# Kernel tuning notes

Hardware: AMD Instinct MI355X
Metric: run time of the kernel (lower is better)

The kernel has to match this reference:

```python
import jax, jax.numpy as jnp
import numpy as np

N = 50000      # nodes
E = 800000     # edges
D_IN, D_H, D_OUT = 256, 256, 128
BN_EPS = 1e-5


def setup_inputs() -> dict:
    key = jax.random.key(0)
    ks = jax.random.split(key, 16)
    inp = {}
    inp["x"] = jax.random.normal(ks[0], (N, D_IN), dtype=jnp.float32)
    inp["edge_index"] = jax.random.randint(ks[1], (2, E), 0, N, dtype=jnp.int32)
    s1 = 1.0 / np.sqrt(D_IN)
    s2 = 1.0 / np.sqrt(D_H)
    inp["W1"] = jax.random.normal(ks[2], (D_IN, D_H), dtype=jnp.float32) * s1
    inp["b1"] = jnp.zeros((D_H,), dtype=jnp.float32)
    inp["g1"] = jnp.ones((D_H,), dtype=jnp.float32)
    inp["be1"] = jnp.zeros((D_H,), dtype=jnp.float32)
    inp["m1"] = jax.random.normal(ks[3], (D_H,), dtype=jnp.float32) * 0.1
    inp["v1"] = jax.random.uniform(ks[4], (D_H,), dtype=jnp.float32, minval=0.5, maxval=1.5)
    inp["W2"] = jax.random.normal(ks[5], (D_H, D_H), dtype=jnp.float32) * s2
    inp["b2"] = jnp.zeros((D_H,), dtype=jnp.float32)
    inp["g2"] = jnp.ones((D_H,), dtype=jnp.float32)
    inp["be2"] = jnp.zeros((D_H,), dtype=jnp.float32)
    inp["m2"] = jax.random.normal(ks[6], (D_H,), dtype=jnp.float32) * 0.1
    inp["v2"] = jax.random.uniform(ks[7], (D_H,), dtype=jnp.float32, minval=0.5, maxval=1.5)
    inp["W3"] = jax.random.normal(ks[8], (D_H, D_OUT), dtype=jnp.float32) * s2
    inp["b3"] = jnp.zeros((D_OUT,), dtype=jnp.float32)
    return inp


def reference(x, edge_index, W1, b1, g1, be1, m1, v1,
              W2, b2, g2, be2, m2, v2, W3, b3):
    # Add self-loops (PyG GCNConv default) and compute symmetric normalization once.
    loop = jnp.arange(N, dtype=edge_index.dtype)
    src = jnp.concatenate([edge_index[0], loop])   # [E+N]
    dst = jnp.concatenate([edge_index[1], loop])   # [E+N]
    deg = jax.ops.segment_sum(jnp.ones_like(dst, dtype=x.dtype), dst, num_segments=N)
    dinv = jax.lax.rsqrt(deg)                      # deg >= 1 thanks to self-loops
    norm = (dinv[src] * dinv[dst])[:, None]        # [E+N, 1]

    def gcn_conv(h, W, b):
        h = h @ W                                   # [N, D]
        agg = jax.ops.segment_sum(h[src] * norm, dst, num_segments=N)
        return agg + b

    def bn_eval(h, g, be, m, v):
        return (h - m) * (g * jax.lax.rsqrt(v + BN_EPS)) + be

    h = jax.nn.relu(bn_eval(gcn_conv(x, W1, b1), g1, be1, m1, v1))  # dropout = identity (eval)
    h = jax.nn.relu(bn_eval(gcn_conv(h, W2, b2), g2, be2, m2, v2))
    out = gcn_conv(h, W3, b3)                       # [N, D_OUT]
    return out
```

## Files before the change

kernel.cpp:

```cpp
#include <hip/hip_runtime.h>
#include <hip/hip_bf16.h>
#include <hip/hip_fp16.h>


#define GN 50000
#define GE 800000

typedef float f32x4 __attribute__((ext_vector_type(4)));
typedef short bf16x8 __attribute__((ext_vector_type(8)));

static __device__ __forceinline__ ushort f2bf_rn(float f) {
    unsigned u = __float_as_uint(f);
    u += 0x7fffu + ((u >> 16) & 1u);
    return (ushort)(u >> 16);
}
static __device__ __forceinline__ float bf2f(ushort h) {
    return __uint_as_float(((unsigned)h) << 16);
}


__global__ __launch_bounds__(256) void init_kernel(int* counts, int* cursor) {
    int i = blockIdx.x * 256 + threadIdx.x;
    if (i < GN) { counts[i] = 0; cursor[i] = 0; }
}

__global__ __launch_bounds__(256) void count_kernel(const int* __restrict__ dst, int* __restrict__ counts) {
    int e = blockIdx.x * 256 + threadIdx.x;
    if (e < GE) atomicAdd(&counts[dst[e]], 1);
}

__global__ __launch_bounds__(256) void dinv_kernel(const int* __restrict__ counts, float* __restrict__ dinv) {
    int i = blockIdx.x * 256 + threadIdx.x;
    if (i < GN) dinv[i] = rsqrtf((float)counts[i] + 1.0f);
}

__global__ __launch_bounds__(1024) void scan_kernel(const int* __restrict__ counts, int* __restrict__ row_ptr) {
    __shared__ int sums[1024];
    int tid = threadIdx.x;
    int chunk = (GN + 1023) / 1024;
    int start = tid * chunk;
    int end = min(start + chunk, GN);
    int s = 0;
    for (int i = start; i < end; i++) s += counts[i];
    sums[tid] = s;
    __syncthreads();
    for (int off = 1; off < 1024; off <<= 1) {
        int v = (tid >= off) ? sums[tid - off] : 0;
        __syncthreads();
        sums[tid] += v;
        __syncthreads();
    }
    int run = (tid == 0) ? 0 : sums[tid - 1];
    for (int i = start; i < end; i++) { row_ptr[i] = run; run += counts[i]; }
    if (tid == 1023) row_ptr[GN] = sums[1023];
}

__global__ __launch_bounds__(256) void fill_kernel(const int* __restrict__ src, const int* __restrict__ dst,
                                                   const int* __restrict__ row_ptr, int* __restrict__ cursor,
                                                   int* __restrict__ col) {
    int e = blockIdx.x * 256 + threadIdx.x;
    if (e < GE) {
        int d = dst[e];
        int pos = row_ptr[d] + atomicAdd(&cursor[d], 1);
        col[pos] = src[e];
    }
}

__global__ __launch_bounds__(256) void params_kernel(
    const float* b1, const float* g1, const float* be1, const float* m1, const float* v1,
    const float* b2, const float* g2, const float* be2, const float* m2, const float* v2,
    float* prm) {
    int t = threadIdx.x;
    float s1 = g1[t] * rsqrtf(v1[t] + 1e-5f);
    prm[0 * 256 + t] = s1;
    prm[1 * 256 + t] = (b1[t] - m1[t]) * s1 + be1[t];
    float s2 = g2[t] * rsqrtf(v2[t] + 1e-5f);
    prm[2 * 256 + t] = s2;
    prm[3 * 256 + t] = (b2[t] - m2[t]) * s2 + be2[t];
}


__global__ __launch_bounds__(256) void conv_split(const float* __restrict__ in, ushort* __restrict__ hi,
                                                  ushort* __restrict__ lo, int n4) {
    int i = blockIdx.x * 256 + threadIdx.x;
    if (i >= n4) return;
    float4 v = *(const float4*)&in[(size_t)i * 4];
    ushort4 h, l;
    h.x = f2bf_rn(v.x); l.x = f2bf_rn(v.x - bf2f(h.x));
    h.y = f2bf_rn(v.y); l.y = f2bf_rn(v.y - bf2f(h.y));
    h.z = f2bf_rn(v.z); l.z = f2bf_rn(v.z - bf2f(h.z));
    h.w = f2bf_rn(v.w); l.w = f2bf_rn(v.w - bf2f(h.w));
    *(ushort4*)&hi[(size_t)i * 4] = h;
    *(ushort4*)&lo[(size_t)i * 4] = l;
}

__global__ __launch_bounds__(256) void transpose_w(const float* __restrict__ W, ushort* __restrict__ hiT,
                                                   ushort* __restrict__ loT, int DO) {
    int idx = blockIdx.x * 256 + threadIdx.x;
    if (idx >= DO * 256) return;
    int n = idx >> 8, k = idx & 255;
    float v = W[k * DO + n];
    ushort h = f2bf_rn(v);
    hiT[idx] = h;
    loT[idx] = f2bf_rn(v - bf2f(h));
}


template <int DO>
__global__ __launch_bounds__(256) void gemm_mfma(const ushort* __restrict__ Ahi, const ushort* __restrict__ Alo,
                                                 const ushort* __restrict__ Bhi, const ushort* __restrict__ Blo,
                                                 const float* __restrict__ dinv, __half* __restrict__ C, int M) {
    __shared__ ushort lds[4][128][40];
    int tid = threadIdx.x;
    int lane = tid & 63;
    int wave = tid >> 6;
    int wm = wave >> 1, wn = wave & 1;
    int m0 = blockIdx.x * 128;
    int n0 = blockIdx.y * 128;
    int rsel = lane & 15;
    int ksel = (lane >> 4) * 8;

    f32x4 acc[4][4] = {};

    for (int k0 = 0; k0 < 256; k0 += 32) {
        auto stage = [&](const ushort* __restrict__ src, int baseRow, int rClamp, int p) {
#pragma unroll
            for (int j = 0; j < 2; j++) {
                int o = (tid + j * 256) * 16;
                int row = o >> 6;
                int kb = o & 63;
                int rg = min(baseRow + row, rClamp);
                uint4 v = *(const uint4*)((const char*)src + (size_t)rg * 512 + (size_t)k0 * 2 + kb);
                *(uint4*)((char*)&lds[p][row][0] + kb) = v;
            }
        };
        stage(Ahi, m0, M - 1, 0);
        stage(Alo, m0, M - 1, 1);
        stage(Bhi, n0, DO - 1, 2);
        stage(Blo, n0, DO - 1, 3);
        __syncthreads();

        bf16x8 bh[4], bl[4];
#pragma unroll
        for (int ni = 0; ni < 4; ni++) {
            bh[ni] = *(const bf16x8*)&lds[2][wn * 64 + ni * 16 + rsel][ksel];
            bl[ni] = *(const bf16x8*)&lds[3][wn * 64 + ni * 16 + rsel][ksel];
        }
#pragma unroll
        for (int mi = 0; mi < 4; mi++) {
            bf16x8 ah = *(const bf16x8*)&lds[0][wm * 64 + mi * 16 + rsel][ksel];
            bf16x8 al = *(const bf16x8*)&lds[1][wm * 64 + mi * 16 + rsel][ksel];
#pragma unroll
            for (int ni = 0; ni < 4; ni++) {
                acc[mi][ni] = __builtin_amdgcn_mfma_f32_16x16x32_bf16(ah, bh[ni], acc[mi][ni], 0, 0, 0);
                acc[mi][ni] = __builtin_amdgcn_mfma_f32_16x16x32_bf16(ah, bl[ni], acc[mi][ni], 0, 0, 0);
                acc[mi][ni] = __builtin_amdgcn_mfma_f32_16x16x32_bf16(al, bh[ni], acc[mi][ni], 0, 0, 0);
            }
        }
        __syncthreads();
    }

#pragma unroll
    for (int mi = 0; mi < 4; mi++) {
#pragma unroll
        for (int j = 0; j < 4; j++) {
            int r = m0 + wm * 64 + mi * 16 + (lane >> 4) * 4 + j;
            if (r < M) {
                float dv = dinv[r];
#pragma unroll
                for (int ni = 0; ni < 4; ni++) {
                    int c = n0 + wn * 64 + ni * 16 + rsel;
                    C[(size_t)r * DO + c] = __float2half_rn(acc[mi][ni][j] * dv);
                }
            }
        }
    }
}

template <int D, int MODE>
__global__ __launch_bounds__(256) void agg_kernel(const __half* __restrict__ Hs, const int* __restrict__ row_ptr,
                                                  const int* __restrict__ col, const float* __restrict__ dinv,
                                                  const float* __restrict__ pa, const float* __restrict__ pc,
                                                  float* __restrict__ outF, ushort* __restrict__ outHi,
                                                  ushort* __restrict__ outLo, int M) {
    constexpr int V = D / 64;
    int w = blockIdx.x * 4 + (threadIdx.x >> 6);
    if (w >= M) return;
    int lane = threadIdx.x & 63;
    const __half* base = Hs + lane * V;
    float acc[V];

    auto addrow = [&](const __half* p) {
        if constexpr (V == 4) {
            __half2 v01 = *(const __half2*)(p);
            __half2 v23 = *(const __half2*)(p + 2);
            float2 f0 = __half22float2(v01);
            float2 f1 = __half22float2(v23);
            acc[0] += f0.x; acc[1] += f0.y; acc[2] += f1.x; acc[3] += f1.y;
        } else {
            __half2 v01 = *(const __half2*)(p);
            float2 f0 = __half22float2(v01);
            acc[0] += f0.x; acc[1] += f0.y;
        }
    };
#pragma unroll
    for (int j = 0; j < V; j++) acc[j] = 0.f;
    addrow(base + (size_t)w * D);

    int e = row_ptr[w], end = row_ptr[w + 1];
    for (; e + 4 <= end; e += 4) {
        int s0 = col[e + 0], s1 = col[e + 1], s2 = col[e + 2], s3 = col[e + 3];
        addrow(base + (size_t)s0 * D);
        addrow(base + (size_t)s1 * D);
        addrow(base + (size_t)s2 * D);
        addrow(base + (size_t)s3 * D);
    }
    for (; e < end; e++) addrow(base + (size_t)col[e] * D);

    float dv = dinv[w];
    if constexpr (MODE == 1) {
        ushort4 h, l;
        float val;
        int d = lane * V;
        val = fmaxf(fmaf(acc[0] * dv, pa[d + 0], pc[d + 0]), 0.f);
        h.x = f2bf_rn(val); l.x = f2bf_rn(val - bf2f(h.x));
        val = fmaxf(fmaf(acc[1] * dv, pa[d + 1], pc[d + 1]), 0.f);
        h.y = f2bf_rn(val); l.y = f2bf_rn(val - bf2f(h.y));
        val = fmaxf(fmaf(acc[2] * dv, pa[d + 2], pc[d + 2]), 0.f);
        h.z = f2bf_rn(val); l.z = f2bf_rn(val - bf2f(h.z));
        val = fmaxf(fmaf(acc[3] * dv, pa[d + 3], pc[d + 3]), 0.f);
        h.w = f2bf_rn(val); l.w = f2bf_rn(val - bf2f(h.w));
        *(ushort4*)&outHi[(size_t)w * D + d] = h;
        *(ushort4*)&outLo[(size_t)w * D + d] = l;
    } else {
#pragma unroll
        for (int j = 0; j < V; j++) {
            int d = lane * V + j;
            outF[(size_t)w * D + d] = acc[j] * dv + pa[d];
        }
    }
}


extern "C" void kernel_launch(void* const* d_in, const int* in_sizes, int n_in,
                              void* d_out, int out_size, void* d_ws, size_t ws_size,
                              hipStream_t stream) {
    const float* x = (const float*)d_in[0];
    const int* ei = (const int*)d_in[1];
    const int* srcIdx = ei;
    const int* dstIdx = ei + GE;
    const float* W1 = (const float*)d_in[2];
    const float* b1 = (const float*)d_in[3];
    const float* g1 = (const float*)d_in[4];
    const float* be1 = (const float*)d_in[5];
    const float* m1 = (const float*)d_in[6];
    const float* v1 = (const float*)d_in[7];
    const float* W2 = (const float*)d_in[8];
    const float* b2 = (const float*)d_in[9];
    const float* g2 = (const float*)d_in[10];
    const float* be2 = (const float*)d_in[11];
    const float* m2 = (const float*)d_in[12];
    const float* v2 = (const float*)d_in[13];
    const float* W3 = (const float*)d_in[14];
    const float* b3 = (const float*)d_in[15];
    float* out = (float*)d_out;

    size_t off = 0;
    char* wsb = (char*)d_ws;
    auto take = [&](size_t bytes) -> char* {
        char* p = wsb + off;
        off += (bytes + 255) & ~(size_t)255;
        return p;
    };
    float* dinv = (float*)take((size_t)GN * 4);
    int* counts = (int*)take((size_t)GN * 4);
    int* cursor = (int*)take((size_t)GN * 4);
    int* row_ptr = (int*)take((size_t)(GN + 1) * 4);
    int* col = (int*)take((size_t)GE * 4);
    float* prm = (float*)take(4 * 256 * 4);
    __half* hH = (__half*)take((size_t)GN * 256 * 2);
    ushort* Phi = (ushort*)take((size_t)GN * 256 * 2);
    ushort* Plo = (ushort*)take((size_t)GN * 256 * 2);
    ushort* WT1h = (ushort*)take(256 * 256 * 2);
    ushort* WT1l = (ushort*)take(256 * 256 * 2);
    ushort* WT2h = (ushort*)take(256 * 256 * 2);
    ushort* WT2l = (ushort*)take(256 * 256 * 2);
    ushort* WT3h = (ushort*)take(128 * 256 * 2);
    ushort* WT3l = (ushort*)take(128 * 256 * 2);

    const float* a1 = prm + 0 * 256;
    const float* c1 = prm + 1 * 256;
    const float* a2 = prm + 2 * 256;
    const float* c2 = prm + 3 * 256;

    int nb = (GN + 255) / 256;
    int eb = (GE + 255) / 256;

    init_kernel<<<nb, 256, 0, stream>>>(counts, cursor);
    count_kernel<<<eb, 256, 0, stream>>>(dstIdx, counts);
    dinv_kernel<<<nb, 256, 0, stream>>>(counts, dinv);
    scan_kernel<<<1, 1024, 0, stream>>>(counts, row_ptr);
    fill_kernel<<<eb, 256, 0, stream>>>(srcIdx, dstIdx, row_ptr, cursor, col);
    params_kernel<<<1, 256, 0, stream>>>(b1, g1, be1, m1, v1, b2, g2, be2, m2, v2, prm);

    int n4 = GN * 64;
    conv_split<<<(n4 + 255) / 256, 256, 0, stream>>>(x, Phi, Plo, n4);
    transpose_w<<<(256 * 256 + 255) / 256, 256, 0, stream>>>(W1, WT1h, WT1l, 256);
    transpose_w<<<(256 * 256 + 255) / 256, 256, 0, stream>>>(W2, WT2h, WT2l, 256);
    transpose_w<<<(128 * 256 + 255) / 256, 256, 0, stream>>>(W3, WT3h, WT3l, 128);

    dim3 gg((GN + 127) / 128, 2);
    dim3 gg3((GN + 127) / 128, 1);
    int ab = (GN + 3) / 4;

    gemm_mfma<256><<<gg, 256, 0, stream>>>(Phi, Plo, WT1h, WT1l, dinv, hH, GN);
    agg_kernel<256, 1><<<ab, 256, 0, stream>>>(hH, row_ptr, col, dinv, a1, c1, nullptr, Phi, Plo, GN);
    gemm_mfma<256><<<gg, 256, 0, stream>>>(Phi, Plo, WT2h, WT2l, dinv, hH, GN);
    agg_kernel<256, 1><<<ab, 256, 0, stream>>>(hH, row_ptr, col, dinv, a2, c2, nullptr, Phi, Plo, GN);
    gemm_mfma<128><<<gg3, 256, 0, stream>>>(Phi, Plo, WT3h, WT3l, dinv, hH, GN);
    agg_kernel<128, 0><<<ab, 256, 0, stream>>>(hH, row_ptr, col, dinv, b3, b3, out, nullptr, nullptr, GN);
}
```

Before: 549.8 us.

## Replace serial scan with atomic segment allocation and batch gathers by eight

Replaces the single-block prefix scan that builds the CSR row pointers with a parallel kernel. Each wavefront scans its counts with shuffles and reserves a contiguous range through an atomic on a global total. Rows therefore get non-sorted but disjoint segments, described by a base and a count. The aggregation kernel now loads eight column indices and then eight neighbor rows before accumulating, so more gathers are in flight per wave. Row segment order now depends on scheduling, which may reduce locality between consecutive nodes but keeps results correct, apart from summation-order differences.

```diff
diff --git a/kernel.cpp b/kernel.cpp
--- a/kernel.cpp
+++ b/kernel.cpp
@@ -19,9 +19,10 @@
 }
 
 
-__global__ __launch_bounds__(256) void init_kernel(int* counts, int* cursor) {
+__global__ __launch_bounds__(256) void init_kernel(int* counts, int* cursor, int* total) {
     int i = blockIdx.x * 256 + threadIdx.x;
     if (i < GN) { counts[i] = 0; cursor[i] = 0; }
+    if (i == 0) *total = 0;
 }
 
 __global__ __launch_bounds__(256) void count_kernel(const int* __restrict__ dst, int* __restrict__ counts) {
@@ -34,34 +35,31 @@
     if (i < GN) dinv[i] = rsqrtf((float)counts[i] + 1.0f);
 }
 
-__global__ __launch_bounds__(1024) void scan_kernel(const int* __restrict__ counts, int* __restrict__ row_ptr) {
-    __shared__ int sums[1024];
-    int tid = threadIdx.x;
-    int chunk = (GN + 1023) / 1024;
-    int start = tid * chunk;
-    int end = min(start + chunk, GN);
-    int s = 0;
-    for (int i = start; i < end; i++) s += counts[i];
-    sums[tid] = s;
-    __syncthreads();
-    for (int off = 1; off < 1024; off <<= 1) {
-        int v = (tid >= off) ? sums[tid - off] : 0;
-        __syncthreads();
-        sums[tid] += v;
-        __syncthreads();
-    }
-    int run = (tid == 0) ? 0 : sums[tid - 1];
-    for (int i = start; i < end; i++) { row_ptr[i] = run; run += counts[i]; }
-    if (tid == 1023) row_ptr[GN] = sums[1023];
+__global__ __launch_bounds__(256) void alloc_kernel(const int* __restrict__ counts, int* __restrict__ base,
+                                                    int* __restrict__ total) {
+    int i = blockIdx.x * 256 + threadIdx.x;
+    int lane = threadIdx.x & 63;
+    int c = (i < GN) ? counts[i] : 0;
+    int v = c;
+#pragma unroll
+    for (int off = 1; off < 64; off <<= 1) {
+        int t = __shfl_up(v, off);
+        if (lane >= off) v += t;
+    }
+    int waveSum = __shfl(v, 63);
+    int wb = 0;
+    if (lane == 63) wb = atomicAdd(total, waveSum);
+    wb = __shfl(wb, 63);
+    if (i < GN) base[i] = wb + v - c;
 }
 
 __global__ __launch_bounds__(256) void fill_kernel(const int* __restrict__ src, const int* __restrict__ dst,
-                                                   const int* __restrict__ row_ptr, int* __restrict__ cursor,
+                                                   const int* __restrict__ base, int* __restrict__ cursor,
                                                    int* __restrict__ col) {
     int e = blockIdx.x * 256 + threadIdx.x;
     if (e < GE) {
         int d = dst[e];
-        int pos = row_ptr[d] + atomicAdd(&cursor[d], 1);
+        int pos = base[d] + atomicAdd(&cursor[d], 1);
         col[pos] = src[e];
     }
 }
@@ -178,8 +176,9 @@
 }
 
 template <int D, int MODE>
-__global__ __launch_bounds__(256) void agg_kernel(const __half* __restrict__ Hs, const int* __restrict__ row_ptr,
-                                                  const int* __restrict__ col, const float* __restrict__ dinv,
+__global__ __launch_bounds__(256) void agg_kernel(const __half* __restrict__ Hs, const int* __restrict__ base,
+                                                  const int* __restrict__ counts, const float* __restrict__ dinv,
+                                                  const int* __restrict__ col,
                                                   const float* __restrict__ pa, const float* __restrict__ pc,
                                                   float* __restrict__ outF, ushort* __restrict__ outHi,
                                                   ushort* __restrict__ outLo, int M) {
@@ -187,35 +186,55 @@
     int w = blockIdx.x * 4 + (threadIdx.x >> 6);
     if (w >= M) return;
     int lane = threadIdx.x & 63;
-    const __half* base = Hs + lane * V;
+    const char* gbase = (const char*)(Hs + lane * V);
     float acc[V];
-
-    auto addrow = [&](const __half* p) {
+#pragma unroll
+    for (int j = 0; j < V; j++) acc[j] = 0.f;
+
+    auto accum32 = [&](unsigned bits, int j2) {
+        __half2 h = *(__half2*)&bits;
+        float2 f = __half22float2(h);
+        acc[j2 + 0] += f.x;
+        acc[j2 + 1] += f.y;
+    };
+
+    if constexpr (V == 4) {
+        uint2 r = *(const uint2*)(gbase + (size_t)w * D * 2);
+        accum32(r.x, 0); accum32(r.y, 2);
+    } else {
+        unsigned r = *(const unsigned*)(gbase + (size_t)w * D * 2);
+        accum32(r, 0);
+    }
+
+    int e = base[w], end = e + counts[w];
+    for (; e + 8 <= end; e += 8) {
+        int idx[8];
+#pragma unroll
+        for (int t = 0; t < 8; t++) idx[t] = col[e + t];
         if constexpr (V == 4) {
-            __half2 v01 = *(const __half2*)(p);
-            __half2 v23 = *(const __half2*)(p + 2);
-            float2 f0 = __half22float2(v01);
-            float2 f1 = __half22float2(v23);
-            acc[0] += f0.x; acc[1] += f0.y; acc[2] += f1.x; acc[3] += f1.y;
+            uint2 r[8];
+#pragma unroll
+            for (int t = 0; t < 8; t++) r[t] = *(const uint2*)(gbase + (size_t)idx[t] * (D * 2));
+#pragma unroll
+            for (int t = 0; t < 8; t++) { accum32(r[t].x, 0); accum32(r[t].y, 2); }
         } else {
-            __half2 v01 = *(const __half2*)(p);
-            float2 f0 = __half22float2(v01);
-            acc[0] += f0.x; acc[1] += f0.y;
-        }
-    };
-#pragma unroll
-    for (int j = 0; j < V; j++) acc[j] = 0.f;
-    addrow(base + (size_t)w * D);
-
-    int e = row_ptr[w], end = row_ptr[w + 1];
-    for (; e + 4 <= end; e += 4) {
-        int s0 = col[e + 0], s1 = col[e + 1], s2 = col[e + 2], s3 = col[e + 3];
-        addrow(base + (size_t)s0 * D);
-        addrow(base + (size_t)s1 * D);
-        addrow(base + (size_t)s2 * D);
-        addrow(base + (size_t)s3 * D);
-    }
-    for (; e < end; e++) addrow(base + (size_t)col[e] * D);
+            unsigned r[8];
+#pragma unroll
+            for (int t = 0; t < 8; t++) r[t] = *(const unsigned*)(gbase + (size_t)idx[t] * (D * 2));
+#pragma unroll
+            for (int t = 0; t < 8; t++) accum32(r[t], 0);
+        }
+    }
+    for (; e < end; e++) {
+        int s = col[e];
+        if constexpr (V == 4) {
+            uint2 r = *(const uint2*)(gbase + (size_t)s * (D * 2));
+            accum32(r.x, 0); accum32(r.y, 2);
+        } else {
+            unsigned r = *(const unsigned*)(gbase + (size_t)s * (D * 2));
+            accum32(r, 0);
+        }
+    }
 
     float dv = dinv[w];
     if constexpr (MODE == 1) {
@@ -275,7 +294,8 @@
     float* dinv = (float*)take((size_t)GN * 4);
     int* counts = (int*)take((size_t)GN * 4);
     int* cursor = (int*)take((size_t)GN * 4);
-    int* row_ptr = (int*)take((size_t)(GN + 1) * 4);
+    int* segbase = (int*)take((size_t)GN * 4);
+    int* total = (int*)take(256);
     int* col = (int*)take((size_t)GE * 4);
     float* prm = (float*)take(4 * 256 * 4);
     __half* hH = (__half*)take((size_t)GN * 256 * 2);
@@ -296,11 +316,11 @@
     int nb = (GN + 255) / 256;
     int eb = (GE + 255) / 256;
 
-    init_kernel<<<nb, 256, 0, stream>>>(counts, cursor);
+    init_kernel<<<nb, 256, 0, stream>>>(counts, cursor, total);
     count_kernel<<<eb, 256, 0, stream>>>(dstIdx, counts);
     dinv_kernel<<<nb, 256, 0, stream>>>(counts, dinv);
-    scan_kernel<<<1, 1024, 0, stream>>>(counts, row_ptr);
-    fill_kernel<<<eb, 256, 0, stream>>>(srcIdx, dstIdx, row_ptr, cursor, col);
+    alloc_kernel<<<nb, 256, 0, stream>>>(counts, segbase, total);
+    fill_kernel<<<eb, 256, 0, stream>>>(srcIdx, dstIdx, segbase, cursor, col);
     params_kernel<<<1, 256, 0, stream>>>(b1, g1, be1, m1, v1, b2, g2, be2, m2, v2, prm);
 
     int n4 = GN * 64;
@@ -314,9 +334,9 @@
     int ab = (GN + 3) / 4;
 
     gemm_mfma<256><<<gg, 256, 0, stream>>>(Phi, Plo, WT1h, WT1l, dinv, hH, GN);
-    agg_kernel<256, 1><<<ab, 256, 0, stream>>>(hH, row_ptr, col, dinv, a1, c1, nullptr, Phi, Plo, GN);
+    agg_kernel<256, 1><<<ab, 256, 0, stream>>>(hH, segbase, counts, dinv, col, a1, c1, nullptr, Phi, Plo, GN);
     gemm_mfma<256><<<gg, 256, 0, stream>>>(Phi, Plo, WT2h, WT2l, dinv, hH, GN);
-    agg_kernel<256, 1><<<ab, 256, 0, stream>>>(hH, row_ptr, col, dinv, a2, c2, nullptr, Phi, Plo, GN);
+    agg_kernel<256, 1><<<ab, 256, 0, stream>>>(hH, segbase, counts, dinv, col, a2, c2, nullptr, Phi, Plo, GN);
     gemm_mfma<128><<<gg3, 256, 0, stream>>>(Phi, Plo, WT3h, WT3l, dinv, hH, GN);
-    agg_kernel<128, 0><<<ab, 256, 0, stream>>>(hH, row_ptr, col, dinv, b3, b3, out, nullptr, nullptr, GN);
-}
+    agg_kernel<128, 0><<<ab, 256, 0, stream>>>(hH, segbase, counts, dinv, col, b3, b3, out, nullptr, nullptr, GN);
+}
```

Measured after the change: 487.5 us. -11.3%, faster.
